# Kernel tuning notes

Hardware: AMD Instinct MI355X
Metric: run time of the kernel (lower is better)

Reference implementation:

```python
import jax, jax.numpy as jnp
import numpy as np

N_NODES = 100000
N_EDGES = 1600000


def setup_inputs() -> dict:
    key = jax.random.key(0)
    ks = jax.random.split(key, 6)
    x = jax.random.normal(ks[0], (N_NODES, 128), dtype=jnp.float32)
    edge_index = jax.random.randint(ks[1], (2, N_EDGES), 0, N_NODES, dtype=jnp.int64)
    # glorot-ish scaled weights
    W0 = jax.random.normal(ks[2], (128, 64), dtype=jnp.float32) * (1.0 / np.sqrt(128))
    W1 = jax.random.normal(ks[3], (64, 64), dtype=jnp.float32) * (1.0 / np.sqrt(64))
    W2 = jax.random.normal(ks[4], (64, 40), dtype=jnp.float32) * (1.0 / np.sqrt(64))
    b0 = jnp.zeros((64,), jnp.float32)
    b1 = jnp.zeros((64,), jnp.float32)
    b2 = jnp.zeros((40,), jnp.float32)
    return {"x": x, "edge_index": edge_index, "W0": W0, "b0": b0,
            "W1": W1, "b1": b1, "W2": W2, "b2": b2}


def _gcn_norm(edge_index, n, dtype):
    # PyG gcn_norm: add self-loops, deg over targets, norm = d^-1/2[src]*d^-1/2[dst]
    loop = jnp.arange(n, dtype=edge_index.dtype)
    src = jnp.concatenate([edge_index[0], loop])
    dst = jnp.concatenate([edge_index[1], loop])
    deg = jax.ops.segment_sum(jnp.ones_like(dst, dtype=dtype), dst, num_segments=n)
    dinv = jnp.where(deg > 0, jax.lax.rsqrt(deg), 0.0)
    return src, dst, dinv[src] * dinv[dst]


def reference(x, edge_index, W0, b0, W1, b1, W2, b2):
    n = x.shape[0]
    src, dst, norm = _gcn_norm(edge_index, n, x.dtype)

    def conv(h, W, b):
        h = h @ W                                   # [N, out]
        msg = h[src] * norm[:, None]                # gather + per-edge scale
        return jax.ops.segment_sum(msg, dst, num_segments=n) + b

    # dropout skipped (eval mode); relu between layers per forward()
    h = jax.nn.relu(conv(x, W0, b0))
    h = jax.nn.relu(conv(h, W1, b1))
    return conv(h, W2, b2)
```

## Files before the change

### kernel.cpp

```cpp
#include <hip/hip_runtime.h>
#include <hip/hip_fp16.h>


#define ALIGN256(x) (((size_t)(x) + 255) & ~(size_t)255)


__global__ __launch_bounds__(256) void k_coarse(const int* __restrict__ ei,
                                                int* __restrict__ ccnt,
                                                int E, int NBUK) {
    __shared__ int h[512];
    int t = threadIdx.x;
    for (int i = t; i < NBUK; i += 256) h[i] = 0;
    __syncthreads();
    int e0 = blockIdx.x * 8192;
    int e1 = min(e0 + 8192, E);
    for (int e = e0 + t; e < e1; e += 256) atomicAdd(&h[ei[E + e] >> 8], 1);
    __syncthreads();
    for (int i = t; i < NBUK; i += 256) {
        int c = h[i];
        if (c) atomicAdd(&ccnt[i], c);
    }
}


__global__ __launch_bounds__(256) void k_cscan(const int* __restrict__ ccnt,
                                               int* __restrict__ cbase,
                                               int* __restrict__ cpos,
                                               int* __restrict__ row_start,
                                               int NBUK, int E, int N) {
    __shared__ int sd[256];
    int t = threadIdx.x;
    int i0 = 2 * t, i1 = 2 * t + 1;
    int v0 = (i0 < NBUK) ? ccnt[i0] : 0;
    int v1 = (i1 < NBUK) ? ccnt[i1] : 0;
    int s = v0 + v1;
    sd[t] = s;
    __syncthreads();
    for (int off = 1; off < 256; off <<= 1) {
        int u = (t >= off) ? sd[t - off] : 0;
        __syncthreads();
        sd[t] += u;
        __syncthreads();
    }
    int base = sd[t] - s;
    if (i0 < NBUK) { cbase[i0] = base;      cpos[i0] = base; }
    if (i1 < NBUK) { cbase[i1] = base + v0; cpos[i1] = base + v0; }
    if (t == 0) { cbase[NBUK] = E; row_start[N] = E; }
}


__global__ __launch_bounds__(256) void k_passA(const int* __restrict__ ei,
                                               int* __restrict__ cpos,
                                               unsigned int* __restrict__ stage,
                                               int E, int NBUK) {
    __shared__ int h[512];
    __shared__ int base[512];
    int t = threadIdx.x;
    for (int i = t; i < NBUK; i += 256) h[i] = 0;
    __syncthreads();
    int e0 = blockIdx.x * 8192;
    int e1 = min(e0 + 8192, E);
    for (int e = e0 + t; e < e1; e += 256) atomicAdd(&h[ei[E + e] >> 8], 1);
    __syncthreads();
    for (int b = t; b < NBUK; b += 256) {
        int c = h[b];
        base[b] = c ? atomicAdd(&cpos[b], c) : 0;
        h[b] = 0;
    }
    __syncthreads();
    for (int e = e0 + t; e < e1; e += 256) {
        unsigned int s = (unsigned int)ei[e];
        int d = ei[E + e];
        int b = d >> 8;
        int off = base[b] + atomicAdd(&h[b], 1);
        stage[off] = ((unsigned int)(d & 255) << 24) | s;
    }
}


__global__ __launch_bounds__(256) void k_B1(const unsigned int* __restrict__ stage,
                                            const int* __restrict__ cbase,
                                            int* __restrict__ row_start,
                                            float* __restrict__ dinv, int N) {
    __shared__ int cnt[256];
    __shared__ int sd[256];
    int b = blockIdx.x;
    int n0 = b << 8;
    int t = threadIdx.x;
    cnt[t] = 0;
    __syncthreads();
    int s0 = cbase[b], s1 = cbase[b + 1];
    for (int j = s0 + t; j < s1; j += 256) atomicAdd(&cnt[stage[j] >> 24], 1);
    __syncthreads();
    int c = cnt[t];
    sd[t] = c;
    __syncthreads();
    for (int off = 1; off < 256; off <<= 1) {
        int u = (t >= off) ? sd[t - off] : 0;
        __syncthreads();
        sd[t] += u;
        __syncthreads();
    }
    int excl = sd[t] - c;
    int node = n0 + t;
    if (node < N) {
        row_start[node] = s0 + excl;
        dinv[node] = 1.0f / sqrtf((float)(c + 1));
    }
}


__global__ __launch_bounds__(256) void k_B2(const unsigned int* __restrict__ stage,
                                            const int* __restrict__ cbase,
                                            const int* __restrict__ row_start,
                                            const float* __restrict__ dinv,
                                            int2* __restrict__ ep, int N) {
    __shared__ int lpos[256];
    __shared__ float ld[256];
    int b = blockIdx.x;
    int n0 = b << 8;
    int t = threadIdx.x;
    int node = n0 + t;
    if (node < N) {
        lpos[t] = row_start[node];
        ld[t] = dinv[node];
    }
    __syncthreads();
    int s0 = cbase[b], s1 = cbase[b + 1];
    for (int j = s0 + t; j < s1; j += 256) {
        unsigned int v = stage[j];
        int li = v >> 24;
        int src = v & 0xFFFFFF;
        int slot = atomicAdd(&lpos[li], 1);
        ep[slot] = make_int2(src, __float_as_int(dinv[src] * ld[li]));
    }
}


template <int K, int OUT>
__global__ __launch_bounds__(256) void k_gemm32(const float* __restrict__ X,
                                                const float* __restrict__ W,
                                                __half* __restrict__ Y, int N) {
    __shared__ float Wl[32 * 64];
    __shared__ float Al[64 * 36];
    int tid = threadIdx.x;
    int tx = tid & 15;
    int ty = tid >> 4;
    int row0 = blockIdx.x * 64;

    float acc[4][4];
#pragma unroll
    for (int i = 0; i < 4; i++)
#pragma unroll
        for (int j = 0; j < 4; j++) acc[i][j] = 0.0f;

    for (int kt = 0; kt < K; kt += 32) {
        __syncthreads();
#pragma unroll
        for (int it = 0; it < 2; it++) {
            int idx = tid + it * 256;
            int k = idx >> 4;
            int c4 = (idx & 15) << 2;
            float4 v = make_float4(0.f, 0.f, 0.f, 0.f);
            if (c4 < OUT) v = *(const float4*)&W[(size_t)(kt + k) * OUT + c4];
            *(float4*)&Wl[k * 64 + c4] = v;
        }
#pragma unroll
        for (int it = 0; it < 2; it++) {
            int vid = tid + it * 256;
            int r = vid >> 3;
            int kk = (vid & 7) << 2;
            int row = row0 + r;
            float4 v = make_float4(0.f, 0.f, 0.f, 0.f);
            if (row < N) v = *(const float4*)&X[(size_t)row * K + kt + kk];
            *(float4*)&Al[r * 36 + kk] = v;
        }
        __syncthreads();
#pragma unroll
        for (int k = 0; k < 32; k += 4) {
            float4 a[4], w[4];
#pragma unroll
            for (int i = 0; i < 4; i++) a[i] = *(const float4*)&Al[(ty + 16 * i) * 36 + k];
#pragma unroll
            for (int j = 0; j < 4; j++) w[j] = *(const float4*)&Wl[(k + j) * 64 + 4 * tx];
#pragma unroll
            for (int i = 0; i < 4; i++) {
                acc[i][0] += a[i].x * w[0].x; acc[i][1] += a[i].x * w[0].y;
                acc[i][2] += a[i].x * w[0].z; acc[i][3] += a[i].x * w[0].w;
                acc[i][0] += a[i].y * w[1].x; acc[i][1] += a[i].y * w[1].y;
                acc[i][2] += a[i].y * w[1].z; acc[i][3] += a[i].y * w[1].w;
                acc[i][0] += a[i].z * w[2].x; acc[i][1] += a[i].z * w[2].y;
                acc[i][2] += a[i].z * w[2].z; acc[i][3] += a[i].z * w[2].w;
                acc[i][0] += a[i].w * w[3].x; acc[i][1] += a[i].w * w[3].y;
                acc[i][2] += a[i].w * w[3].z; acc[i][3] += a[i].w * w[3].w;
            }
        }
    }

    int c0 = 4 * tx;
#pragma unroll
    for (int i = 0; i < 4; i++) {
        int row = row0 + ty + 16 * i;
        if (row < N && c0 + 4 <= OUT) {
            __half2 p0 = __floats2half2_rn(acc[i][0], acc[i][1]);
            __half2 p1 = __floats2half2_rn(acc[i][2], acc[i][3]);
            uint2 pk = make_uint2(*(unsigned int*)&p0, *(unsigned int*)&p1);
            *(uint2*)&Y[(size_t)row * OUT + c0] = pk;
        }
    }
}


template <int OUT>
__global__ __launch_bounds__(256) void k_gemm16(const __half* __restrict__ X,
                                                const float* __restrict__ W,
                                                __half* __restrict__ Y, int N) {
    __shared__ float Wl[32 * 64];
    __shared__ float Al[64 * 36];
    int tid = threadIdx.x;
    int tx = tid & 15;
    int ty = tid >> 4;
    int row0 = blockIdx.x * 64;

    float acc[4][4];
#pragma unroll
    for (int i = 0; i < 4; i++)
#pragma unroll
        for (int j = 0; j < 4; j++) acc[i][j] = 0.0f;

    for (int kt = 0; kt < 64; kt += 32) {
        __syncthreads();
#pragma unroll
        for (int it = 0; it < 2; it++) {
            int idx = tid + it * 256;
            int k = idx >> 4;
            int c4 = (idx & 15) << 2;
            float4 v = make_float4(0.f, 0.f, 0.f, 0.f);
            if (c4 < OUT) v = *(const float4*)&W[(size_t)(kt + k) * OUT + c4];
            *(float4*)&Wl[k * 64 + c4] = v;
        }
#pragma unroll
        for (int it = 0; it < 2; it++) {
            int vid = tid + it * 256;
            int r = vid >> 3;
            int kk = (vid & 7) << 2;
            int row = row0 + r;
            uint2 hv = make_uint2(0, 0);
            if (row < N) hv = *(const uint2*)&X[(size_t)row * 64 + kt + kk];
            __half2* hp = (__half2*)&hv;
            float2 f0 = __half22float2(hp[0]);
            float2 f1 = __half22float2(hp[1]);
            *(float4*)&Al[r * 36 + kk] = make_float4(f0.x, f0.y, f1.x, f1.y);
        }
        __syncthreads();
#pragma unroll
        for (int k = 0; k < 32; k += 4) {
            float4 a[4], w[4];
#pragma unroll
            for (int i = 0; i < 4; i++) a[i] = *(const float4*)&Al[(ty + 16 * i) * 36 + k];
#pragma unroll
            for (int j = 0; j < 4; j++) w[j] = *(const float4*)&Wl[(k + j) * 64 + 4 * tx];
#pragma unroll
            for (int i = 0; i < 4; i++) {
                acc[i][0] += a[i].x * w[0].x; acc[i][1] += a[i].x * w[0].y;
                acc[i][2] += a[i].x * w[0].z; acc[i][3] += a[i].x * w[0].w;
                acc[i][0] += a[i].y * w[1].x; acc[i][1] += a[i].y * w[1].y;
                acc[i][2] += a[i].y * w[1].z; acc[i][3] += a[i].y * w[1].w;
                acc[i][0] += a[i].z * w[2].x; acc[i][1] += a[i].z * w[2].y;
                acc[i][2] += a[i].z * w[2].z; acc[i][3] += a[i].z * w[2].w;
                acc[i][0] += a[i].w * w[3].x; acc[i][1] += a[i].w * w[3].y;
                acc[i][2] += a[i].w * w[3].z; acc[i][3] += a[i].w * w[3].w;
            }
        }
    }

    int c0 = 4 * tx;
#pragma unroll
    for (int i = 0; i < 4; i++) {
        int row = row0 + ty + 16 * i;
        if (row < N && c0 + 4 <= OUT) {
            __half2 p0 = __floats2half2_rn(acc[i][0], acc[i][1]);
            __half2 p1 = __floats2half2_rn(acc[i][2], acc[i][3]);
            uint2 pk = make_uint2(*(unsigned int*)&p0, *(unsigned int*)&p1);
            *(uint2*)&Y[(size_t)row * OUT + c0] = pk;
        }
    }
}


__device__ __forceinline__ void fma8(float4& a0, float4& a1, uint4 hv, float w) {
    __half2* hp = (__half2*)&hv;
    float2 f0 = __half22float2(hp[0]);
    float2 f1 = __half22float2(hp[1]);
    float2 f2 = __half22float2(hp[2]);
    float2 f3 = __half22float2(hp[3]);
    a0.x += f0.x * w; a0.y += f0.y * w; a0.z += f1.x * w; a0.w += f1.y * w;
    a1.x += f2.x * w; a1.y += f2.y * w; a1.z += f3.x * w; a1.w += f3.y * w;
}

template <int NV, int F, int RELU, typename OutT>
__global__ __launch_bounds__(256) void k_agg(const __half* __restrict__ H,
                                             const int* __restrict__ row_start,
                                             const int2* __restrict__ ep,
                                             const float* __restrict__ dinv,
                                             const float* __restrict__ bias,
                                             OutT* __restrict__ out, int N) {
    int tid = threadIdx.x;
    int lane = tid & 63;
    int sub = lane >> 3;
    int lq = lane & 7;
    int node = blockIdx.x * 32 + (tid >> 6) * 8 + sub;
    if (node >= N) return;
    const bool act = (NV == 8) || (lq < NV);

    int jb = row_start[node];
    int je = row_start[node + 1];
    float dv = dinv[node];

    float4 a0 = make_float4(0.f, 0.f, 0.f, 0.f);
    float4 a1 = make_float4(0.f, 0.f, 0.f, 0.f);
    if (act) {
        uint4 hv = *(const uint4*)&H[(size_t)node * F + 8 * lq];
        fma8(a0, a1, hv, dv * dv);
    }

    int j = jb;
    for (; j + 8 <= je; j += 8) {
        int2 e0 = ep[j],     e1 = ep[j + 1], e2 = ep[j + 2], e3 = ep[j + 3];
        int2 e4 = ep[j + 4], e5 = ep[j + 5], e6 = ep[j + 6], e7 = ep[j + 7];
        if (act) {
            uint4 h0 = *(const uint4*)&H[(size_t)e0.x * F + 8 * lq];
            uint4 h1 = *(const uint4*)&H[(size_t)e1.x * F + 8 * lq];
            uint4 h2 = *(const uint4*)&H[(size_t)e2.x * F + 8 * lq];
            uint4 h3 = *(const uint4*)&H[(size_t)e3.x * F + 8 * lq];
            uint4 h4 = *(const uint4*)&H[(size_t)e4.x * F + 8 * lq];
            uint4 h5 = *(const uint4*)&H[(size_t)e5.x * F + 8 * lq];
            uint4 h6 = *(const uint4*)&H[(size_t)e6.x * F + 8 * lq];
            uint4 h7 = *(const uint4*)&H[(size_t)e7.x * F + 8 * lq];
            fma8(a0, a1, h0, __int_as_float(e0.y));
            fma8(a0, a1, h1, __int_as_float(e1.y));
            fma8(a0, a1, h2, __int_as_float(e2.y));
            fma8(a0, a1, h3, __int_as_float(e3.y));
            fma8(a0, a1, h4, __int_as_float(e4.y));
            fma8(a0, a1, h5, __int_as_float(e5.y));
            fma8(a0, a1, h6, __int_as_float(e6.y));
            fma8(a0, a1, h7, __int_as_float(e7.y));
        }
    }
    for (; j + 2 <= je; j += 2) {
        int2 e0 = ep[j], e1 = ep[j + 1];
        if (act) {
            uint4 h0 = *(const uint4*)&H[(size_t)e0.x * F + 8 * lq];
            uint4 h1 = *(const uint4*)&H[(size_t)e1.x * F + 8 * lq];
            fma8(a0, a1, h0, __int_as_float(e0.y));
            fma8(a0, a1, h1, __int_as_float(e1.y));
        }
    }
    if (j < je) {
        int2 e = ep[j];
        if (act) {
            uint4 h = *(const uint4*)&H[(size_t)e.x * F + 8 * lq];
            fma8(a0, a1, h, __int_as_float(e.y));
        }
    }

    if (act) {
        float4 b0 = *(const float4*)&bias[8 * lq];
        float4 b1 = *(const float4*)&bias[8 * lq + 4];
        a0.x += b0.x; a0.y += b0.y; a0.z += b0.z; a0.w += b0.w;
        a1.x += b1.x; a1.y += b1.y; a1.z += b1.z; a1.w += b1.w;
        if (RELU) {
            a0.x = fmaxf(a0.x, 0.f); a0.y = fmaxf(a0.y, 0.f);
            a0.z = fmaxf(a0.z, 0.f); a0.w = fmaxf(a0.w, 0.f);
            a1.x = fmaxf(a1.x, 0.f); a1.y = fmaxf(a1.y, 0.f);
            a1.z = fmaxf(a1.z, 0.f); a1.w = fmaxf(a1.w, 0.f);
        }
        if constexpr (sizeof(OutT) == 2) {
            __half2 p0 = __floats2half2_rn(a0.x, a0.y);
            __half2 p1 = __floats2half2_rn(a0.z, a0.w);
            __half2 p2 = __floats2half2_rn(a1.x, a1.y);
            __half2 p3 = __floats2half2_rn(a1.z, a1.w);
            uint4 pk = make_uint4(*(unsigned int*)&p0, *(unsigned int*)&p1,
                                  *(unsigned int*)&p2, *(unsigned int*)&p3);
            *(uint4*)&out[(size_t)node * F + 8 * lq] = pk;
        } else {
            *(float4*)&out[(size_t)node * F + 8 * lq] = a0;
            *(float4*)&out[(size_t)node * F + 8 * lq + 4] = a1;
        }
    }
}


extern "C" void kernel_launch(void* const* d_in, const int* in_sizes, int n_in,
                              void* d_out, int out_size, void* d_ws, size_t ws_size,
                              hipStream_t stream) {
    const float* x  = (const float*)d_in[0];
    const int*   ei = (const int*)d_in[1];
    const float* W0 = (const float*)d_in[2];
    const float* b0 = (const float*)d_in[3];
    const float* W1 = (const float*)d_in[4];
    const float* b1 = (const float*)d_in[5];
    const float* W2 = (const float*)d_in[6];
    const float* b2 = (const float*)d_in[7];
    float* out = (float*)d_out;

    const int N = in_sizes[0] / 128;
    const int E = in_sizes[1] / 2;
    const int NBUK = (N + 255) >> 8;

    char* w = (char*)d_ws;
    size_t off = 0;
    int*    ccnt      = (int*)(w + off);    off = ALIGN256(off + (size_t)NBUK * 4);
    int*    cbase     = (int*)(w + off);    off = ALIGN256(off + (size_t)(NBUK + 1) * 4);
    int*    cpos      = (int*)(w + off);    off = ALIGN256(off + (size_t)NBUK * 4);
    int*    row_start = (int*)(w + off);    off = ALIGN256(off + (size_t)(N + 1) * 4);
    float*  dinv      = (float*)(w + off);  off = ALIGN256(off + (size_t)N * 4);
    int2*   ep        = (int2*)(w + off);   off = ALIGN256(off + (size_t)E * 8);
    __half* bufH      = (__half*)(w + off); off = ALIGN256(off + (size_t)N * 64 * 2);
    __half* bufG      = (__half*)(w + off); off = ALIGN256(off + (size_t)N * 64 * 2);
    unsigned int* stage = (unsigned int*)bufG;

    const int gGemm = (N + 63) / 64;
    const int gAgg  = (N + 31) / 32;
    const int gPA   = (E + 8191) / 8192;

    hipMemsetAsync(ccnt, 0, (size_t)NBUK * 4, stream);
    k_gemm32<128, 64><<<gGemm, 256, 0, stream>>>(x, W0, bufH, N);
    k_coarse<<<gPA, 256, 0, stream>>>(ei, ccnt, E, NBUK);
    k_cscan<<<1, 256, 0, stream>>>(ccnt, cbase, cpos, row_start, NBUK, E, N);
    k_passA<<<gPA, 256, 0, stream>>>(ei, cpos, stage, E, NBUK);
    k_B1<<<NBUK, 256, 0, stream>>>(stage, cbase, row_start, dinv, N);
    k_B2<<<NBUK, 256, 0, stream>>>(stage, cbase, row_start, dinv, ep, N);

    k_agg<8, 64, 1, __half><<<gAgg, 256, 0, stream>>>(bufH, row_start, ep, dinv, b0, bufG, N);
    k_gemm16<64><<<gGemm, 256, 0, stream>>>(bufG, W1, bufH, N);
    k_agg<8, 64, 1, __half><<<gAgg, 256, 0, stream>>>(bufH, row_start, ep, dinv, b1, bufG, N);
    k_gemm16<40><<<gGemm, 256, 0, stream>>>(bufG, W2, bufH, N);
    k_agg<5, 40, 0, float><<<gAgg, 256, 0, stream>>>(bufH, row_start, ep, dinv, b2, out, N);
}
```

Measured before the change: 325.8 us.

## Replace FP32 SIMT GEMMs with MFMA f16 matrix-core GEMM kernel

Replaces the two shared-memory FP32 tiled GEMM kernels with a single templated kernel that uses the 16x16x32 f16 MFMA instruction. Weights are converted to f16 and pre-swizzled into LDS, and each wave computes 16 rows directly from global memory. The aim is to cut ALU-bound time in the three dense transforms. In exchange, the first layer's input and weights are rounded to f16 before the multiply, which slightly reduces precision.

```diff
diff --git a/kernel.cpp b/kernel.cpp
--- a/kernel.cpp
+++ b/kernel.cpp
@@ -3,6 +3,10 @@
 
 
 #define ALIGN256(x) (((size_t)(x) + 255) & ~(size_t)255)
+
+typedef _Float16 f16;
+typedef f16 f16x8 __attribute__((ext_vector_type(8)));
+typedef float f32x4 __attribute__((ext_vector_type(4)));
 
 
 __global__ __launch_bounds__(256) void k_coarse(const int* __restrict__ ei,
@@ -137,152 +141,69 @@
 }
 
 
-template <int K, int OUT>
-__global__ __launch_bounds__(256) void k_gemm32(const float* __restrict__ X,
-                                                const float* __restrict__ W,
-                                                __half* __restrict__ Y, int N) {
-    __shared__ float Wl[32 * 64];
-    __shared__ float Al[64 * 36];
+template <int K, int OUT, int NF, typename XT>
+__global__ __launch_bounds__(256) void k_mgemm(const XT* __restrict__ X,
+                                               const float* __restrict__ W,
+                                               __half* __restrict__ Y, int N) {
+    constexpr int NC = NF * 16;
+    constexpr int NT = K / 32;
+    __shared__ f16 Wl[NT * NF * 4 * 128];
+
     int tid = threadIdx.x;
-    int tx = tid & 15;
-    int ty = tid >> 4;
-    int row0 = blockIdx.x * 64;
-
-    float acc[4][4];
-#pragma unroll
-    for (int i = 0; i < 4; i++)
-#pragma unroll
-        for (int j = 0; j < 4; j++) acc[i][j] = 0.0f;
-
-    for (int kt = 0; kt < K; kt += 32) {
-        __syncthreads();
-#pragma unroll
-        for (int it = 0; it < 2; it++) {
-            int idx = tid + it * 256;
-            int k = idx >> 4;
-            int c4 = (idx & 15) << 2;
-            float4 v = make_float4(0.f, 0.f, 0.f, 0.f);
-            if (c4 < OUT) v = *(const float4*)&W[(size_t)(kt + k) * OUT + c4];
-            *(float4*)&Wl[k * 64 + c4] = v;
-        }
-#pragma unroll
-        for (int it = 0; it < 2; it++) {
-            int vid = tid + it * 256;
-            int r = vid >> 3;
-            int kk = (vid & 7) << 2;
-            int row = row0 + r;
-            float4 v = make_float4(0.f, 0.f, 0.f, 0.f);
-            if (row < N) v = *(const float4*)&X[(size_t)row * K + kt + kk];
-            *(float4*)&Al[r * 36 + kk] = v;
-        }
-        __syncthreads();
-#pragma unroll
-        for (int k = 0; k < 32; k += 4) {
-            float4 a[4], w[4];
-#pragma unroll
-            for (int i = 0; i < 4; i++) a[i] = *(const float4*)&Al[(ty + 16 * i) * 36 + k];
-#pragma unroll
-            for (int j = 0; j < 4; j++) w[j] = *(const float4*)&Wl[(k + j) * 64 + 4 * tx];
-#pragma unroll
-            for (int i = 0; i < 4; i++) {
-                acc[i][0] += a[i].x * w[0].x; acc[i][1] += a[i].x * w[0].y;
-                acc[i][2] += a[i].x * w[0].z; acc[i][3] += a[i].x * w[0].w;
-                acc[i][0] += a[i].y * w[1].x; acc[i][1] += a[i].y * w[1].y;
-                acc[i][2] += a[i].y * w[1].z; acc[i][3] += a[i].y * w[1].w;
-                acc[i][0] += a[i].z * w[2].x; acc[i][1] += a[i].z * w[2].y;
-                acc[i][2] += a[i].z * w[2].z; acc[i][3] += a[i].z * w[2].w;
-                acc[i][0] += a[i].w * w[3].x; acc[i][1] += a[i].w * w[3].y;
-                acc[i][2] += a[i].w * w[3].z; acc[i][3] += a[i].w * w[3].w;
+    for (int idx = tid; idx < K * NC; idx += 256) {
+        int k = idx / NC;
+        int n = idx - k * NC;
+        float v = (n < OUT) ? W[k * OUT + n] : 0.0f;
+        int t = k >> 5, h = (k >> 3) & 3, j = k & 7, f = n >> 4, nn = n & 15;
+        Wl[((t * NF + f) * 4 + h) * 128 + nn * 8 + j] = (f16)v;
+    }
+    __syncthreads();
+
+    int lane = tid & 63;
+    int wid = tid >> 6;
+    int h = lane >> 4;
+    int nn = lane & 15;
+    int row = blockIdx.x * 64 + (wid << 4) + nn;
+    bool valid = row < N;
+
+    f32x4 acc[NF];
+#pragma unroll
+    for (int f = 0; f < NF; ++f) acc[f] = (f32x4){0.f, 0.f, 0.f, 0.f};
+
+#pragma unroll
+    for (int t = 0; t < NT; ++t) {
+        f16x8 xf;
+        if (valid) {
+            if constexpr (sizeof(XT) == 4) {
+                const float* xp = (const float*)X + (size_t)row * K + (t << 5) + (h << 3);
+                float4 u0 = *(const float4*)xp;
+                float4 u1 = *(const float4*)(xp + 4);
+                xf[0] = (f16)u0.x; xf[1] = (f16)u0.y; xf[2] = (f16)u0.z; xf[3] = (f16)u0.w;
+                xf[4] = (f16)u1.x; xf[5] = (f16)u1.y; xf[6] = (f16)u1.z; xf[7] = (f16)u1.w;
+            } else {
+                xf = *(const f16x8*)((const __half*)X + (size_t)row * K + (t << 5) + (h << 3));
             }
-        }
-    }
-
-    int c0 = 4 * tx;
-#pragma unroll
-    for (int i = 0; i < 4; i++) {
-        int row = row0 + ty + 16 * i;
-        if (row < N && c0 + 4 <= OUT) {
-            __half2 p0 = __floats2half2_rn(acc[i][0], acc[i][1]);
-            __half2 p1 = __floats2half2_rn(acc[i][2], acc[i][3]);
-            uint2 pk = make_uint2(*(unsigned int*)&p0, *(unsigned int*)&p1);
-            *(uint2*)&Y[(size_t)row * OUT + c0] = pk;
-        }
-    }
-}
-
-
-template <int OUT>
-__global__ __launch_bounds__(256) void k_gemm16(const __half* __restrict__ X,
-                                                const float* __restrict__ W,
-                                                __half* __restrict__ Y, int N) {
-    __shared__ float Wl[32 * 64];
-    __shared__ float Al[64 * 36];
-    int tid = threadIdx.x;
-    int tx = tid & 15;
-    int ty = tid >> 4;
-    int row0 = blockIdx.x * 64;
-
-    float acc[4][4];
-#pragma unroll
-    for (int i = 0; i < 4; i++)
-#pragma unroll
-        for (int j = 0; j < 4; j++) acc[i][j] = 0.0f;
-
-    for (int kt = 0; kt < 64; kt += 32) {
-        __syncthreads();
-#pragma unroll
-        for (int it = 0; it < 2; it++) {
-            int idx = tid + it * 256;
-            int k = idx >> 4;
-            int c4 = (idx & 15) << 2;
-            float4 v = make_float4(0.f, 0.f, 0.f, 0.f);
-            if (c4 < OUT) v = *(const float4*)&W[(size_t)(kt + k) * OUT + c4];
-            *(float4*)&Wl[k * 64 + c4] = v;
-        }
-#pragma unroll
-        for (int it = 0; it < 2; it++) {
-            int vid = tid + it * 256;
-            int r = vid >> 3;
-            int kk = (vid & 7) << 2;
-            int row = row0 + r;
-            uint2 hv = make_uint2(0, 0);
-            if (row < N) hv = *(const uint2*)&X[(size_t)row * 64 + kt + kk];
-            __half2* hp = (__half2*)&hv;
-            float2 f0 = __half22float2(hp[0]);
-            float2 f1 = __half22float2(hp[1]);
-            *(float4*)&Al[r * 36 + kk] = make_float4(f0.x, f0.y, f1.x, f1.y);
-        }
-        __syncthreads();
-#pragma unroll
-        for (int k = 0; k < 32; k += 4) {
-            float4 a[4], w[4];
-#pragma unroll
-            for (int i = 0; i < 4; i++) a[i] = *(const float4*)&Al[(ty + 16 * i) * 36 + k];
-#pragma unroll
-            for (int j = 0; j < 4; j++) w[j] = *(const float4*)&Wl[(k + j) * 64 + 4 * tx];
-#pragma unroll
-            for (int i = 0; i < 4; i++) {
-                acc[i][0] += a[i].x * w[0].x; acc[i][1] += a[i].x * w[0].y;
-                acc[i][2] += a[i].x * w[0].z; acc[i][3] += a[i].x * w[0].w;
-                acc[i][0] += a[i].y * w[1].x; acc[i][1] += a[i].y * w[1].y;
-                acc[i][2] += a[i].y * w[1].z; acc[i][3] += a[i].y * w[1].w;
-                acc[i][0] += a[i].z * w[2].x; acc[i][1] += a[i].z * w[2].y;
-                acc[i][2] += a[i].z * w[2].z; acc[i][3] += a[i].z * w[2].w;
-                acc[i][0] += a[i].w * w[3].x; acc[i][1] += a[i].w * w[3].y;
-                acc[i][2] += a[i].w * w[3].z; acc[i][3] += a[i].w * w[3].w;
+        } else {
+#pragma unroll
+            for (int j = 0; j < 8; ++j) xf[j] = (f16)0.f;
+        }
+#pragma unroll
+        for (int f = 0; f < NF; ++f) {
+            f16x8 wf = *(const f16x8*)&Wl[((t * NF + f) * 4 + h) * 128 + nn * 8];
+            acc[f] = __builtin_amdgcn_mfma_f32_16x16x32_f16(wf, xf, acc[f], 0, 0, 0);
+        }
+    }
+
+    if (valid) {
+#pragma unroll
+        for (int f = 0; f < NF; ++f) {
+            int c = (f << 4) + (h << 2);
+            if (c < OUT) {
+                __half2 p0 = __floats2half2_rn(acc[f][0], acc[f][1]);
+                __half2 p1 = __floats2half2_rn(acc[f][2], acc[f][3]);
+                uint2 pk = make_uint2(*(unsigned int*)&p0, *(unsigned int*)&p1);
+                *(uint2*)&Y[(size_t)row * OUT + c] = pk;
             }
-        }
-    }
-
-    int c0 = 4 * tx;
-#pragma unroll
-    for (int i = 0; i < 4; i++) {
-        int row = row0 + ty + 16 * i;
-        if (row < N && c0 + 4 <= OUT) {
-            __half2 p0 = __floats2half2_rn(acc[i][0], acc[i][1]);
-            __half2 p1 = __floats2half2_rn(acc[i][2], acc[i][3]);
-            uint2 pk = make_uint2(*(unsigned int*)&p0, *(unsigned int*)&p1);
-            *(uint2*)&Y[(size_t)row * OUT + c0] = pk;
         }
     }
 }
@@ -425,7 +346,7 @@
     const int gPA   = (E + 8191) / 8192;
 
     hipMemsetAsync(ccnt, 0, (size_t)NBUK * 4, stream);
-    k_gemm32<128, 64><<<gGemm, 256, 0, stream>>>(x, W0, bufH, N);
+    k_mgemm<128, 64, 4><<<gGemm, 256, 0, stream>>>(x, W0, bufH, N);
     k_coarse<<<gPA, 256, 0, stream>>>(ei, ccnt, E, NBUK);
     k_cscan<<<1, 256, 0, stream>>>(ccnt, cbase, cpos, row_start, NBUK, E, N);
     k_passA<<<gPA, 256, 0, stream>>>(ei, cpos, stage, E, NBUK);
@@ -433,8 +354,8 @@
     k_B2<<<NBUK, 256, 0, stream>>>(stage, cbase, row_start, dinv, ep, N);
 
     k_agg<8, 64, 1, __half><<<gAgg, 256, 0, stream>>>(bufH, row_start, ep, dinv, b0, bufG, N);
-    k_gemm16<64><<<gGemm, 256, 0, stream>>>(bufG, W1, bufH, N);
+    k_mgemm<64, 64, 4><<<gGemm, 256, 0, stream>>>(bufG, W1, bufH, N);
     k_agg<8, 64, 1, __half><<<gAgg, 256, 0, stream>>>(bufH, row_start, ep, dinv, b1, bufG, N);
-    k_gemm16<40><<<gGemm, 256, 0, stream>>>(bufG, W2, bufH, N);
+    k_mgemm<64, 40, 3><<<gGemm, 256, 0, stream>>>(bufG, W2, bufH, N);
     k_agg<5, 40, 0, float><<<gAgg, 256, 0, stream>>>(bufH, row_start, ep, dinv, b2, out, N);
 }
```

New measurement: 304.8 us. 1.07x faster.
